# Performance work log

Hardware: AMD Instinct MI355X
Metric: run time of the kernel (lower is better)

Reference implementation:

```python
import jax, jax.numpy as jnp
import numpy as np
from jax import lax

K = 3  # kernel_size
PAD = K // 2

def setup_inputs() -> dict:
    key = jax.random.key(0)
    ks = jax.random.split(key, 8)
    B, C, H, W = 8, 96, 128, 128
    x = jax.random.normal(ks[0], (B, C, H, W), dtype=jnp.float32)
    s = 0.05
    dw_w = jax.random.normal(ks[1], (C, 1, 3, 3), dtype=jnp.float32) * s   # depthwise 3x3
    dw_b = jax.random.normal(ks[2], (C,), dtype=jnp.float32) * s
    pw1_w = jax.random.normal(ks[3], (C // 2, C), dtype=jnp.float32) * s   # 1x1: C -> C/2
    pw1_b = jax.random.normal(ks[4], (C // 2,), dtype=jnp.float32) * s
    pw2_w = jax.random.normal(ks[5], (K * K, C // 2), dtype=jnp.float32) * s  # 1x1: C/2 -> 9
    pw2_b = jax.random.normal(ks[6], (K * K,), dtype=jnp.float32) * s
    return {"x": x, "dw_w": dw_w, "dw_b": dw_b, "pw1_w": pw1_w,
            "pw1_b": pw1_b, "pw2_w": pw2_w, "pw2_b": pw2_b}

def _unfold3x3(x):
    # x: (B,C,H,W) -> patches (B,C,9,H,W), index order (di*3+dj) matching F.unfold
    B, C, H, W = x.shape
    xp = jnp.pad(x, ((0, 0), (0, 0), (PAD, PAD), (PAD, PAD)))
    return jnp.stack([xp[:, :, i:i + H, j:j + W] for i in range(K) for j in range(K)], axis=2)

def _forward(x, dw_w, dw_b, pw1_w, pw1_b, pw2_w, pw2_b):
    B, C, H, W = x.shape
    # kernel predictor: depthwise 3x3 -> 1x1 -> leaky_relu(0.2) -> 1x1
    h = lax.conv_general_dilated(x, dw_w, (1, 1), ((PAD, PAD), (PAD, PAD)),
                                 dimension_numbers=("NCHW", "OIHW", "NCHW"),
                                 feature_group_count=C)
    h = h + dw_b[None, :, None, None]
    h = jnp.einsum("bchw,oc->bohw", h, pw1_w) + pw1_b[None, :, None, None]
    h = jnp.where(h >= 0, h, 0.2 * h)  # LeakyReLU(0.2)
    kw = jnp.einsum("bchw,oc->bohw", h, pw2_w) + pw2_b[None, :, None, None]  # (B,9,H,W)
    kw = jax.nn.softmax(kw, axis=1)
    patches = _unfold3x3(x)                      # (B,C,9,H,W)
    x_smooth = jnp.einsum("bckhw,bkhw->bchw", patches, kw)
    return x_smooth

def reference(x, dw_w, dw_b, pw1_w, pw1_b, pw2_w, pw2_b):
    return _forward(x, dw_w, dw_b, pw1_w, pw1_b, pw2_w, pw2_b)
```

## Files before the change

kernel.cpp:

```cpp
#include <hip/hip_runtime.h>
#include <math.h>

#define Cc 96
#define Hh 128
#define Ww 128
#define HWsz (Hh*Ww)
#define TW 16
#define TH 8
#define LROW 18
#define LPLANE 180
#define CPAD 104

typedef _Float16 h2 __attribute__((ext_vector_type(2)));
typedef short    s8v __attribute__((ext_vector_type(8)));
typedef float    f4v __attribute__((ext_vector_type(4)));

__device__ __forceinline__ unsigned pkrtz_u(float a, float b) {
    return __builtin_bit_cast(unsigned, __builtin_amdgcn_cvt_pkrtz(a, b));
}
__device__ __forceinline__ h2 pk2(float a, float b) {
    return __builtin_bit_cast(h2, __builtin_amdgcn_cvt_pkrtz(a, b));
}
__device__ __forceinline__ h2 u2h(unsigned u) { return __builtin_bit_cast(h2, u); }
__device__ __forceinline__ unsigned cvt_pk_bf16(float lo, float hi) {
    unsigned r;
    asm("v_cvt_pk_bf16_f32 %0, %1, %2" : "=v"(r) : "v"(lo), "v"(hi));
    return r;
}

__host__ __device__ __forceinline__ unsigned f2bf(float f) {
    unsigned u = __float_as_uint(f);
    return (u + 0x7fffu + ((u >> 16) & 1u)) >> 16;
}

#define GETW(v, wi) ((wi)==0 ? (v).x : (wi)==1 ? (v).y : (wi)==2 ? (v).z : (v).w)

#define OFF_WDW 0
#define OFF_W2  480
#define OFF_P1B 704
#define OFF_A   768
#define NPK     3072
#define WLDS_N  752

__global__ void alpf_prep(const float* __restrict__ dw_w, const float* __restrict__ dw_b,
                          const float* __restrict__ pw1_w, const float* __restrict__ pw1_b,
                          const float* __restrict__ pw2_w, unsigned* __restrict__ wpk)
{
    int i = blockIdx.x * 256 + threadIdx.x;
    if (i >= NPK) return;
    unsigned v = 0u;
    if (i < OFF_W2) {
        int g = i / 120, rem = i % 120, ks = rem / 40, s = rem % 40;
        int chb = 32*ks + 8*g;
        if (s < 4) v = pkrtz_u(dw_b[chb + 2*s], dw_b[chb + 2*s + 1]);
        else { int t = (s - 4) / 4, d = (s - 4) % 4;
               v = pkrtz_u(dw_w[(chb + 2*d)*9 + t], dw_w[(chb + 2*d + 1)*9 + t]); }
    } else if (i < OFF_P1B) {
        int idx = i - OFF_W2; int g = idx / 56, s = idx % 56;
        if (s < 54) { int k = s / 6, mm = s % 6, m = mm / 2, rp = mm % 2;
            int o = 16*m + 4*g + 2*rp;
            v = pkrtz_u(pw2_w[k*48 + o], pw2_w[k*48 + o + 1]); }
    } else if (i < OFF_P1B + 48) {
        v = __float_as_uint(pw1_b[i - OFF_P1B]);
    } else if (i >= OFF_A) {
        int idx = i - OFF_A; int f = idx / 256, rem = idx % 256, l = rem / 4, d = rem % 4;
        int m = f / 3, ks = f % 3;
        int o  = 16*m + (l & 15);
        int ch = 32*ks + 8*(l >> 4) + 2*d;
        v = f2bf(pw1_w[o*Cc + ch]) | (f2bf(pw1_w[o*Cc + ch + 1]) << 16);
    }
    wpk[i] = v;
}

__global__ __launch_bounds__(128, 2)
void alpf_fused(const float* __restrict__ x,
                const float* __restrict__ pw2_b,
                const unsigned* __restrict__ wpk,
                float* __restrict__ out)
{
    __shared__ unsigned short lx[LPLANE * CPAD];
    __shared__ unsigned wlds[WLDS_N];

    const int tid = threadIdx.x;

    const int nwg   = gridDim.x;
    const int chunk = nwg >> 3;
    const int logical = (blockIdx.x & 7) * chunk + (blockIdx.x >> 3);
    const int tx = logical & 7;
    const int ty = (logical >> 3) & 15;
    const int b  = logical >> 7;
    const int x0 = tx * TW;
    const int y0 = ty * TH;
    const float* __restrict__ xb = x + (size_t)b * Cc * HWsz;

    *reinterpret_cast<uint4*>(&wlds[tid * 4]) =
        *reinterpret_cast<const uint4*>(wpk + tid * 4);
    if (tid < 60)
        *reinterpret_cast<uint4*>(&wlds[512 + tid * 4]) =
            *reinterpret_cast<const uint4*>(wpk + 512 + tid * 4);

    const int lane = tid & 63;
    const int g    = lane >> 4;
    const int c15  = lane & 15;
    const int w    = tid >> 6;

    s8v Af[9];
    #pragma unroll
    for (int f = 0; f < 9; ++f)
        Af[f] = __builtin_bit_cast(s8v,
            *reinterpret_cast<const uint4*>(wpk + OFF_A + (f*64 + lane)*4));

    const int e1 = tid;
    const int r1 = e1 / LROW, q1 = e1 - r1 * LROW;
    const int gy1 = y0 - 1 + r1, gx1 = x0 - 1 + q1;
    const bool ok1 = (gy1 >= 0) & (gy1 < Hh) & (gx1 >= 0) & (gx1 < Ww);
    const int g1 = gy1 * Ww + gx1;
    const int e2 = tid + 128;
    const bool v2 = (e2 < LPLANE);
    const int r2 = e2 / LROW, q2 = e2 - r2 * LROW;
    const int gy2 = y0 - 1 + r2, gx2 = x0 - 1 + q2;
    const bool ok2 = v2 & (gy2 >= 0) & (gy2 < Hh) & (gx2 >= 0) & (gx2 < Ww);
    const int g2 = gy2 * Ww + gx2;

    #pragma unroll 2
    for (int cg = 0; cg < 12; ++cg) {
        const int c0 = cg * 8;
        const float* xc = xb + (size_t)c0 * HWsz;
        {
            float v0 = ok1 ? xc[0*HWsz + g1] : 0.f;
            float v1 = ok1 ? xc[1*HWsz + g1] : 0.f;
            float v2_ = ok1 ? xc[2*HWsz + g1] : 0.f;
            float v3 = ok1 ? xc[3*HWsz + g1] : 0.f;
            float v4 = ok1 ? xc[4*HWsz + g1] : 0.f;
            float v5 = ok1 ? xc[5*HWsz + g1] : 0.f;
            float v6 = ok1 ? xc[6*HWsz + g1] : 0.f;
            float v7 = ok1 ? xc[7*HWsz + g1] : 0.f;
            *reinterpret_cast<uint4*>(&lx[e1 * CPAD + c0]) =
                make_uint4(pkrtz_u(v0,v1), pkrtz_u(v2_,v3), pkrtz_u(v4,v5), pkrtz_u(v6,v7));
        }
        if (v2) {
            float v0 = ok2 ? xc[0*HWsz + g2] : 0.f;
            float v1 = ok2 ? xc[1*HWsz + g2] : 0.f;
            float v2_ = ok2 ? xc[2*HWsz + g2] : 0.f;
            float v3 = ok2 ? xc[3*HWsz + g2] : 0.f;
            float v4 = ok2 ? xc[4*HWsz + g2] : 0.f;
            float v5 = ok2 ? xc[5*HWsz + g2] : 0.f;
            float v6 = ok2 ? xc[6*HWsz + g2] : 0.f;
            float v7 = ok2 ? xc[7*HWsz + g2] : 0.f;
            *reinterpret_cast<uint4*>(&lx[e2 * CPAD + c0]) =
                make_uint4(pkrtz_u(v0,v1), pkrtz_u(v2_,v3), pkrtz_u(v4,v5), pkrtz_u(v6,v7));
        }
    }
    __syncthreads();

    f4v acc[3][4];
    #pragma unroll
    for (int m = 0; m < 3; ++m) {
        const f4v bb = *reinterpret_cast<const f4v*>(&wlds[OFF_P1B + 16*m + 4*g]);
        #pragma unroll
        for (int n = 0; n < 4; ++n) acc[m][n] = bb;
    }

    #pragma unroll
    for (int ks = 0; ks < 3; ++ks) {
        const int base = (g*3 + ks) * 40;
        const uint4 wb = *reinterpret_cast<const uint4*>(&wlds[base]);
        uint4 wt[9];
        #pragma unroll
        for (int t = 0; t < 9; ++t)
            wt[t] = *reinterpret_cast<const uint4*>(&wlds[base + 4 + 4*t]);
        #pragma unroll
        for (int n = 0; n < 4; ++n) {
            h2 b0 = u2h(wb.x), b1 = u2h(wb.y), b2 = u2h(wb.z), b3 = u2h(wb.w);
            #pragma unroll
            for (int t = 0; t < 9; ++t) {
                const int dy = t / 3, dx = t - 3*dy;
                const uint4 xv = *reinterpret_cast<const uint4*>(
                    &lx[((4*w + n + dy)*LROW + c15 + dx)*CPAD + 32*ks + 8*g]);
                b0 = __builtin_elementwise_fma(u2h(xv.x), u2h(wt[t].x), b0);
                b1 = __builtin_elementwise_fma(u2h(xv.y), u2h(wt[t].y), b1);
                b2 = __builtin_elementwise_fma(u2h(xv.z), u2h(wt[t].z), b2);
                b3 = __builtin_elementwise_fma(u2h(xv.w), u2h(wt[t].w), b3);
            }
            uint4 bq;
            bq.x = cvt_pk_bf16((float)b0.x, (float)b0.y);
            bq.y = cvt_pk_bf16((float)b1.x, (float)b1.y);
            bq.z = cvt_pk_bf16((float)b2.x, (float)b2.y);
            bq.w = cvt_pk_bf16((float)b3.x, (float)b3.y);
            const s8v Bf = __builtin_bit_cast(s8v, bq);
            acc[0][n] = __builtin_amdgcn_mfma_f32_16x16x32_bf16(Af[0 + ks], Bf, acc[0][n], 0, 0, 0);
            acc[1][n] = __builtin_amdgcn_mfma_f32_16x16x32_bf16(Af[3 + ks], Bf, acc[1][n], 0, 0, 0);
            acc[2][n] = __builtin_amdgcn_mfma_f32_16x16x32_bf16(Af[6 + ks], Bf, acc[2][n], 0, 0, 0);
        }
    }

    h2 tpk[4][3][2];
    #pragma unroll
    for (int n = 0; n < 4; ++n)
        #pragma unroll
        for (int m = 0; m < 3; ++m)
            #pragma unroll
            for (int rp = 0; rp < 2; ++rp) {
                float a = acc[m][n][2*rp], c = acc[m][n][2*rp + 1];
                a = (a >= 0.f) ? a : 0.2f * a;
                c = (c >= 0.f) ? c : 0.2f * c;
                tpk[n][m][rp] = pk2(a, c);
            }

    uint4 w2q[14];
    #pragma unroll
    for (int j = 0; j < 14; ++j)
        w2q[j] = *reinterpret_cast<const uint4*>(&wlds[OFF_W2 + g*56 + 4*j]);

    float kwr[4][9];
    #pragma unroll
    for (int k = 0; k < 9; ++k) {
        #pragma unroll
        for (int n = 0; n < 4; ++n) {
            h2 s = pk2(0.f, 0.f);
            #pragma unroll
            for (int m = 0; m < 3; ++m)
                #pragma unroll
                for (int rp = 0; rp < 2; ++rp) {
                    const int d = k*6 + 2*m + rp;
                    s = __builtin_elementwise_fma(tpk[n][m][rp],
                                                  u2h(GETW(w2q[d >> 2], d & 3)), s);
                }
            kwr[n][k] = (float)s.x + (float)s.y;
        }
    }
    #pragma unroll
    for (int n = 0; n < 4; ++n)
        #pragma unroll
        for (int k = 0; k < 9; ++k) {
            float v = kwr[n][k];
            v += __shfl_xor(v, 16);
            v += __shfl_xor(v, 32);
            kwr[n][k] = v + pw2_b[k];
        }

    float kw[9];
    #pragma unroll
    for (int k = 0; k < 9; ++k)
        kw[k] = (g == 0) ? kwr[0][k] : (g == 1) ? kwr[1][k] : (g == 2) ? kwr[2][k] : kwr[3][k];

    float mx = kw[0];
    #pragma unroll
    for (int k = 1; k < 9; ++k) mx = fmaxf(mx, kw[k]);
    float sum = 0.f;
    #pragma unroll
    for (int k = 0; k < 9; ++k) { kw[k] = __expf(kw[k] - mx); sum += kw[k]; }
    const float inv = 1.f / sum;
    h2 kwp[9];
    #pragma unroll
    for (int k = 0; k < 9; ++k) { kw[k] *= inv; kwp[k] = pk2(kw[k], kw[k]); }

    const int sx = c15;
    const int sy = g + 4*w;
    const unsigned short* lb = &lx[(sy * LROW + sx) * CPAD];
    float* __restrict__ ob = out + (size_t)b * Cc * HWsz + (size_t)(y0 + sy) * Ww + (x0 + sx);
    #pragma unroll 2
    for (int cg = 0; cg < 12; ++cg) {
        const int c0 = cg * 8;
        uint4 tp[9];
        #pragma unroll
        for (int k = 0; k < 9; ++k) {
            const int dy = k / 3, dx = k - 3 * dy;
            tp[k] = *reinterpret_cast<const uint4*>(&lb[(dy*LROW + dx)*CPAD + c0]);
        }
        #pragma unroll
        for (int l = 0; l < 4; ++l) {
            h2 a0 = u2h(GETW(tp[0], l)) * kwp[0];
            h2 a1 = u2h(GETW(tp[1], l)) * kwp[1];
            h2 a2 = u2h(GETW(tp[2], l)) * kwp[2];
            a0 = __builtin_elementwise_fma(u2h(GETW(tp[3], l)), kwp[3], a0);
            a1 = __builtin_elementwise_fma(u2h(GETW(tp[4], l)), kwp[4], a1);
            a2 = __builtin_elementwise_fma(u2h(GETW(tp[5], l)), kwp[5], a2);
            a0 = __builtin_elementwise_fma(u2h(GETW(tp[6], l)), kwp[6], a0);
            a1 = __builtin_elementwise_fma(u2h(GETW(tp[7], l)), kwp[7], a1);
            a2 = __builtin_elementwise_fma(u2h(GETW(tp[8], l)), kwp[8], a2);
            float olo = (float)a0.x + (float)a1.x + (float)a2.x;
            float ohi = (float)a0.y + (float)a1.y + (float)a2.y;
            ob[(size_t)(c0 + 2*l)     * HWsz] = olo;
            ob[(size_t)(c0 + 2*l + 1) * HWsz] = ohi;
        }
    }
}

extern "C" void kernel_launch(void* const* d_in, const int* in_sizes, int n_in,
                              void* d_out, int out_size, void* d_ws, size_t ws_size,
                              hipStream_t stream)
{
    const float* x     = (const float*)d_in[0];
    const float* dw_w  = (const float*)d_in[1];
    const float* dw_b  = (const float*)d_in[2];
    const float* pw1_w = (const float*)d_in[3];
    const float* pw1_b = (const float*)d_in[4];
    const float* pw2_w = (const float*)d_in[5];
    const float* pw2_b = (const float*)d_in[6];
    float* outp = (float*)d_out;
    unsigned* wpk = (unsigned*)d_ws;

    alpf_prep<<<(NPK + 255) / 256, 256, 0, stream>>>(dw_w, dw_b, pw1_w, pw1_b, pw2_w, wpk);

    const int B = in_sizes[0] / (Cc * HWsz);
    dim3 grid((Ww / TW) * (Hh / TH) * B);
    alpf_fused<<<grid, 128, 0, stream>>>(x, pw2_b, wpk, outp);
}
```

Before: 39.14 us.

## Double threads per block and split row and channel work across four waves

Raises the block from 128 to 256 threads (4 waves) over the same 16x8 tile. Each thread now loads at most one halo pixel, each wave handles 2 rows in the MFMA stage, and the output stage splits channels into two halves of 48 per lane group. The aim is more parallelism and latency hiding per tile, with fewer registers per thread for accumulators. The cost is more wave scheduling overhead and redundant per-wave weight fragment loads, and occupancy now depends on fitting 4 blocks of 256 threads per CU.

```diff
diff --git a/kernel.cpp b/kernel.cpp
--- a/kernel.cpp
+++ b/kernel.cpp
@@ -72,7 +72,7 @@
     wpk[i] = v;
 }
 
-__global__ __launch_bounds__(128, 2)
+__global__ __launch_bounds__(256, 4)
 void alpf_fused(const float* __restrict__ x,
                 const float* __restrict__ pw2_b,
                 const unsigned* __restrict__ wpk,
@@ -93,16 +93,14 @@
     const int y0 = ty * TH;
     const float* __restrict__ xb = x + (size_t)b * Cc * HWsz;
 
-    *reinterpret_cast<uint4*>(&wlds[tid * 4]) =
-        *reinterpret_cast<const uint4*>(wpk + tid * 4);
-    if (tid < 60)
-        *reinterpret_cast<uint4*>(&wlds[512 + tid * 4]) =
-            *reinterpret_cast<const uint4*>(wpk + 512 + tid * 4);
+    if (tid < 188)
+        *reinterpret_cast<uint4*>(&wlds[tid * 4]) =
+            *reinterpret_cast<const uint4*>(wpk + tid * 4);
 
     const int lane = tid & 63;
     const int g    = lane >> 4;
     const int c15  = lane & 15;
-    const int w    = tid >> 6;
+    const int wv   = tid >> 6;
 
     s8v Af[9];
     #pragma unroll
@@ -110,23 +108,15 @@
         Af[f] = __builtin_bit_cast(s8v,
             *reinterpret_cast<const uint4*>(wpk + OFF_A + (f*64 + lane)*4));
 
-    const int e1 = tid;
-    const int r1 = e1 / LROW, q1 = e1 - r1 * LROW;
-    const int gy1 = y0 - 1 + r1, gx1 = x0 - 1 + q1;
-    const bool ok1 = (gy1 >= 0) & (gy1 < Hh) & (gx1 >= 0) & (gx1 < Ww);
-    const int g1 = gy1 * Ww + gx1;
-    const int e2 = tid + 128;
-    const bool v2 = (e2 < LPLANE);
-    const int r2 = e2 / LROW, q2 = e2 - r2 * LROW;
-    const int gy2 = y0 - 1 + r2, gx2 = x0 - 1 + q2;
-    const bool ok2 = v2 & (gy2 >= 0) & (gy2 < Hh) & (gx2 >= 0) & (gx2 < Ww);
-    const int g2 = gy2 * Ww + gx2;
-
-    #pragma unroll 2
-    for (int cg = 0; cg < 12; ++cg) {
-        const int c0 = cg * 8;
-        const float* xc = xb + (size_t)c0 * HWsz;
-        {
+    if (tid < LPLANE) {
+        const int r1 = tid / LROW, q1 = tid - r1 * LROW;
+        const int gy1 = y0 - 1 + r1, gx1 = x0 - 1 + q1;
+        const bool ok1 = (gy1 >= 0) & (gy1 < Hh) & (gx1 >= 0) & (gx1 < Ww);
+        const int g1 = gy1 * Ww + gx1;
+        #pragma unroll 2
+        for (int cg = 0; cg < 12; ++cg) {
+            const int c0 = cg * 8;
+            const float* xc = xb + (size_t)c0 * HWsz;
             float v0 = ok1 ? xc[0*HWsz + g1] : 0.f;
             float v1 = ok1 ? xc[1*HWsz + g1] : 0.f;
             float v2_ = ok1 ? xc[2*HWsz + g1] : 0.f;
@@ -135,30 +125,18 @@
             float v5 = ok1 ? xc[5*HWsz + g1] : 0.f;
             float v6 = ok1 ? xc[6*HWsz + g1] : 0.f;
             float v7 = ok1 ? xc[7*HWsz + g1] : 0.f;
-            *reinterpret_cast<uint4*>(&lx[e1 * CPAD + c0]) =
+            *reinterpret_cast<uint4*>(&lx[tid * CPAD + c0]) =
                 make_uint4(pkrtz_u(v0,v1), pkrtz_u(v2_,v3), pkrtz_u(v4,v5), pkrtz_u(v6,v7));
         }
-        if (v2) {
-            float v0 = ok2 ? xc[0*HWsz + g2] : 0.f;
-            float v1 = ok2 ? xc[1*HWsz + g2] : 0.f;
-            float v2_ = ok2 ? xc[2*HWsz + g2] : 0.f;
-            float v3 = ok2 ? xc[3*HWsz + g2] : 0.f;
-            float v4 = ok2 ? xc[4*HWsz + g2] : 0.f;
-            float v5 = ok2 ? xc[5*HWsz + g2] : 0.f;
-            float v6 = ok2 ? xc[6*HWsz + g2] : 0.f;
-            float v7 = ok2 ? xc[7*HWsz + g2] : 0.f;
-            *reinterpret_cast<uint4*>(&lx[e2 * CPAD + c0]) =
-                make_uint4(pkrtz_u(v0,v1), pkrtz_u(v2_,v3), pkrtz_u(v4,v5), pkrtz_u(v6,v7));
-        }
     }
     __syncthreads();
 
-    f4v acc[3][4];
+    f4v acc[3][2];
     #pragma unroll
     for (int m = 0; m < 3; ++m) {
         const f4v bb = *reinterpret_cast<const f4v*>(&wlds[OFF_P1B + 16*m + 4*g]);
-        #pragma unroll
-        for (int n = 0; n < 4; ++n) acc[m][n] = bb;
+        acc[m][0] = bb;
+        acc[m][1] = bb;
     }
 
     #pragma unroll
@@ -170,13 +148,13 @@
         for (int t = 0; t < 9; ++t)
             wt[t] = *reinterpret_cast<const uint4*>(&wlds[base + 4 + 4*t]);
         #pragma unroll
-        for (int n = 0; n < 4; ++n) {
+        for (int n = 0; n < 2; ++n) {
             h2 b0 = u2h(wb.x), b1 = u2h(wb.y), b2 = u2h(wb.z), b3 = u2h(wb.w);
             #pragma unroll
             for (int t = 0; t < 9; ++t) {
                 const int dy = t / 3, dx = t - 3*dy;
                 const uint4 xv = *reinterpret_cast<const uint4*>(
-                    &lx[((4*w + n + dy)*LROW + c15 + dx)*CPAD + 32*ks + 8*g]);
+                    &lx[((2*wv + n + dy)*LROW + c15 + dx)*CPAD + 32*ks + 8*g]);
                 b0 = __builtin_elementwise_fma(u2h(xv.x), u2h(wt[t].x), b0);
                 b1 = __builtin_elementwise_fma(u2h(xv.y), u2h(wt[t].y), b1);
                 b2 = __builtin_elementwise_fma(u2h(xv.z), u2h(wt[t].z), b2);
@@ -194,9 +172,9 @@
         }
     }
 
-    h2 tpk[4][3][2];
-    #pragma unroll
-    for (int n = 0; n < 4; ++n)
+    h2 tpk[2][3][2];
+    #pragma unroll
+    for (int n = 0; n < 2; ++n)
         #pragma unroll
         for (int m = 0; m < 3; ++m)
             #pragma unroll
@@ -212,11 +190,11 @@
     for (int j = 0; j < 14; ++j)
         w2q[j] = *reinterpret_cast<const uint4*>(&wlds[OFF_W2 + g*56 + 4*j]);
 
-    float kwr[4][9];
+    float kwr[2][9];
     #pragma unroll
     for (int k = 0; k < 9; ++k) {
         #pragma unroll
-        for (int n = 0; n < 4; ++n) {
+        for (int n = 0; n < 2; ++n) {
             h2 s = pk2(0.f, 0.f);
             #pragma unroll
             for (int m = 0; m < 3; ++m)
@@ -230,7 +208,7 @@
         }
     }
     #pragma unroll
-    for (int n = 0; n < 4; ++n)
+    for (int n = 0; n < 2; ++n)
         #pragma unroll
         for (int k = 0; k < 9; ++k) {
             float v = kwr[n][k];
@@ -239,10 +217,13 @@
             kwr[n][k] = v + pw2_b[k];
         }
 
+    const int nn  = (lane >> 4) & 1;
+    const int chh = lane >> 5;
+    const int row = 2*wv + nn;
+
     float kw[9];
     #pragma unroll
-    for (int k = 0; k < 9; ++k)
-        kw[k] = (g == 0) ? kwr[0][k] : (g == 1) ? kwr[1][k] : (g == 2) ? kwr[2][k] : kwr[3][k];
+    for (int k = 0; k < 9; ++k) kw[k] = nn ? kwr[1][k] : kwr[0][k];
 
     float mx = kw[0];
     #pragma unroll
@@ -255,13 +236,11 @@
     #pragma unroll
     for (int k = 0; k < 9; ++k) { kw[k] *= inv; kwp[k] = pk2(kw[k], kw[k]); }
 
-    const int sx = c15;
-    const int sy = g + 4*w;
-    const unsigned short* lb = &lx[(sy * LROW + sx) * CPAD];
-    float* __restrict__ ob = out + (size_t)b * Cc * HWsz + (size_t)(y0 + sy) * Ww + (x0 + sx);
+    const unsigned short* lb = &lx[(row * LROW + c15) * CPAD];
+    float* __restrict__ ob = out + (size_t)b * Cc * HWsz + (size_t)(y0 + row) * Ww + (x0 + c15);
     #pragma unroll 2
-    for (int cg = 0; cg < 12; ++cg) {
-        const int c0 = cg * 8;
+    for (int cg = 0; cg < 6; ++cg) {
+        const int c0 = chh * 48 + cg * 8;
         uint4 tp[9];
         #pragma unroll
         for (int k = 0; k < 9; ++k) {
@@ -305,5 +284,5 @@
 
     const int B = in_sizes[0] / (Cc * HWsz);
     dim3 grid((Ww / TW) * (Hh / TH) * B);
-    alpf_fused<<<grid, 128, 0, stream>>>(x, pw2_b, wpk, outp);
-}
+    alpf_fused<<<grid, 256, 0, stream>>>(x, pw2_b, wpk, outp);
+}
```

New measurement: 38.25 us. -2.3%, faster.
